# Kernel tuning notes

Measured on AMD Instinct MI355X. Metric: run time of the kernel, lower is better.

## Reference

```python
import jax, jax.numpy as jnp
import numpy as np

N = 4096; B = 32; LATENT = 16; UNITS = 64; NNZ = 65536; K = 2; M = 2 * K + 1

def _spmm(rows, cols, vals, x):
    # sparse [N,N] @ dense [N,FB] via gather + segment_sum
    return jax.ops.segment_sum(vals[:, None] * x[cols], rows, num_segments=N)

def _gconv(y, supports, W, b):
    # y: (B, N*F) -> Chebyshev-style diffusion over each support, then dense projection
    F = y.shape[1] // N
    x0 = y.reshape(B, N, F).transpose(1, 2, 0).reshape(N, F * B)
    xs = [x0]
    for rows, cols, vals in supports:
        x1 = _spmm(rows, cols, vals, x0)
        xs.append(x1)
        xk1, xk2 = x1, x0
        for _ in range(2, K + 1):
            x2 = 2.0 * _spmm(rows, cols, vals, xk1) - xk2
            xs.append(x2)
            xk1, xk2 = x2, xk1
    # [M,N,F,B] -> [B,N,F,M] -> [B*N, F*M], matching torch permute/reshape
    x = jnp.stack(xs).reshape(M, N, F, B).transpose(3, 1, 2, 0).reshape(B * N, F * M)
    return (x @ W + b).reshape(B, N * W.shape[1])

def setup_inputs():
    key = jax.random.key(0)
    ks = jax.random.split(key, 8)
    r = jax.random.randint(ks[0], (NNZ,), 0, N)
    c = jax.random.randint(ks[1], (NNZ,), 0, N)
    v = jax.random.uniform(ks[2], (NNZ,)) + 0.1
    d_row = jax.ops.segment_sum(v, r, num_segments=N)
    d_col = jax.ops.segment_sum(v, c, num_segments=N)
    inv_row = jnp.where(d_row > 0, 1.0 / d_row, 0.0)
    inv_col = jnp.where(d_col > 0, 1.0 / d_col, 0.0)
    # support1 = (D_out^{-1} A)^T ; support2 = (D_in^{-1} A^T)^T  (COO triples)
    s1_rows, s1_cols, s1_vals = c, r, v * inv_row[r]
    s2_rows, s2_cols, s2_vals = r, c, v * inv_col[c]
    def xavier(k, shape):
        scale = np.sqrt(2.0 / (shape[0] + shape[1])).astype(np.float32)
        return jax.random.normal(k, shape, dtype=jnp.float32) * scale
    return {
        "t_local": 0,
        "y": jax.random.normal(ks[3], (B, N * LATENT), dtype=jnp.float32),
        "W_theta": xavier(ks[4], (LATENT * M, LATENT)),
        "b_lat": jnp.ones((LATENT,), jnp.float32),  # bias_start=1.0; shared (LayerParams keys biases by length)
        "W_hid": xavier(ks[5], (LATENT * M, UNITS)),
        "b_hid": jnp.zeros((UNITS,), jnp.float32),
        "W_out": xavier(ks[6], (UNITS * M, LATENT)),
        "s1_rows": s1_rows, "s1_cols": s1_cols, "s1_vals": s1_vals,
        "s2_rows": s2_rows, "s2_cols": s2_cols, "s2_vals": s2_vals,
    }

def reference(t_local, y, W_theta, b_lat, W_hid, b_hid, W_out,
              s1_rows, s1_cols, s1_vals, s2_rows, s2_cols, s2_vals):
    supports = [(s1_rows, s1_cols, s1_vals), (s2_rows, s2_cols, s2_vals)]
    theta = jax.nn.sigmoid(_gconv(y, supports, W_theta, b_lat))
    c = jnp.tanh(_gconv(y, supports, W_hid, b_hid))   # gen_layers = 1
    c = jnp.tanh(_gconv(c, supports, W_out, b_lat))   # shared bias of length latent_dim
    return -theta * c
```

## Files before the change

kernel.cpp:

```cpp
#include <hip/hip_runtime.h>
#include <stdint.h>

#define NN    4096
#define BB    32
#define NNZE  65536
#define WA    512
#define WD    512

typedef __attribute__((ext_vector_type(8))) short bf16x8;
typedef __attribute__((ext_vector_type(4))) float f32x4;

__device__ __forceinline__ float bf2f_lo(unsigned int u) {
    union { unsigned int x; float f; } c; c.x = u << 16; return c.f;
}
__device__ __forceinline__ float bf2f_hi(unsigned int u) {
    union { unsigned int x; float f; } c; c.x = u & 0xffff0000u; return c.f;
}
__device__ __forceinline__ float bf2f(unsigned int h) {
    union { unsigned int u; float f; } c; c.u = h << 16; return c.f;
}
__device__ __forceinline__ unsigned int f2bf(float f) {
    union { float ff; unsigned int u; } c; c.ff = f;
    return (c.u + 0x7fffu + ((c.u >> 16) & 1u)) >> 16;
}

__global__ void hist2_kernel(const int* __restrict__ r1, const int* __restrict__ r2,
                             int* __restrict__ cnt1, int* __restrict__ cnt2) {
    int e = blockIdx.x * blockDim.x + threadIdx.x;
    if (e < NNZE) atomicAdd(&cnt1[r1[e]], 1);
    else          atomicAdd(&cnt2[r2[e - NNZE]], 1);
}

__global__ void scan2_kernel(int* cur1, int* rp1, int* cur2, int* rp2) {
    int* cur = (blockIdx.x == 0) ? cur1 : cur2;
    int* rp  = (blockIdx.x == 0) ? rp1  : rp2;
    __shared__ int part[256];
    int t = threadIdx.x;
    int base = t * 16;
    int loc[16];
    int s = 0;
#pragma unroll
    for (int i = 0; i < 16; ++i) { loc[i] = s; s += cur[base + i]; }
    part[t] = s;
    __syncthreads();
    for (int off = 1; off < 256; off <<= 1) {
        int v = 0;
        if (t >= off) v = part[t - off];
        __syncthreads();
        part[t] += v;
        __syncthreads();
    }
    int excl = (t == 0) ? 0 : part[t - 1];
#pragma unroll
    for (int i = 0; i < 16; ++i) rp[base + i] = excl + loc[i];
    __syncthreads();
#pragma unroll
    for (int i = 0; i < 16; ++i) cur[base + i] = rp[base + i];
    if (t == 255) rp[4096] = part[255];
}

__global__ void util_kernel(const int* __restrict__ r1, const int* __restrict__ c1, const float* __restrict__ v1,
                            const int* __restrict__ r2, const int* __restrict__ c2, const float* __restrict__ v2,
                            int* __restrict__ cur1, int* __restrict__ cur2,
                            int2* __restrict__ ep1, int2* __restrict__ ep2,
                            const float* __restrict__ y, unsigned short* __restrict__ x0h,
                            const float* __restrict__ Wtheta, const float* __restrict__ Whid,
                            const float* __restrict__ Wout,
                            unsigned short* __restrict__ wpa, unsigned short* __restrict__ wpo) {
    int blk = blockIdx.x, t = threadIdx.x;
    if (blk < 512) {
        int e = blk * 256 + t;
        if (e < NNZE) {
            int pos = atomicAdd(&cur1[r1[e]], 1);
            ep1[pos] = make_int2(c1[e], __float_as_int(v1[e]));
        } else {
            int ee = e - NNZE;
            int pos = atomicAdd(&cur2[r2[ee]], 1);
            ep2[pos] = make_int2(c2[ee], __float_as_int(v2[ee]));
        }
    } else if (blk < 2560) {
        int n = (blk - 512) * 2 + (t >> 7);
        int tt = t & 127;
        int b = tt & 31, q = tt >> 5;
        float4 y4 = *(const float4*)(y + (size_t)b * (NN * 16) + n * 16 + 4 * q);
        uint2 o;
        o.x = f2bf(y4.x) | (f2bf(y4.y) << 16);
        o.y = f2bf(y4.z) | (f2bf(y4.w) << 16);
        *(uint2*)(x0h + (size_t)n * WA + b * 16 + 4 * q) = o;
    } else {
        for (int i = t; i < 80 * 104; i += 256) {
            int col = i / 104, k = i - col * 104;
            float v = 0.f;
            if (k < 96) {
                int m = k >> 4, f = k & 15;
                if (m < 5) {
                    float w0, w2, w4, wm;
                    if (col < 16) {
                        w0 = Wtheta[(f * 5 + 0) * 16 + col];
                        w2 = Wtheta[(f * 5 + 2) * 16 + col];
                        w4 = Wtheta[(f * 5 + 4) * 16 + col];
                        wm = Wtheta[(f * 5 + m) * 16 + col];
                    } else {
                        int cc = col - 16;
                        w0 = Whid[(f * 5 + 0) * 64 + cc];
                        w2 = Whid[(f * 5 + 2) * 64 + cc];
                        w4 = Whid[(f * 5 + 4) * 64 + cc];
                        wm = Whid[(f * 5 + m) * 64 + cc];
                    }
                    v = (m == 0) ? w0 - w2 - w4 : (m == 2) ? 2.f * w2 : (m == 4) ? 2.f * w4 : wm;
                }
            }
            wpa[i] = (unsigned short)f2bf(v);
        }
        for (int i = t; i < 80 * 72; i += 256) {
            int col = i / 72, k = i - col * 72;
            float v = 0.f;
            if (k < 64) { int m = col >> 4, up = col & 15; v = Wout[(k * 5 + m) * 16 + up]; }
            wpo[i] = (unsigned short)f2bf(v);
        }
    }
}

__device__ __forceinline__ void gather_wave(const unsigned short* __restrict__ in,
                                            int beg, int end, const int2* __restrict__ ep,
                                            int lane, int* scol, float* sval, float* acc) {
    for (int i0 = beg; i0 < end; i0 += 64) {
        if (i0 + lane < end) { int2 e = ep[i0 + lane]; scol[lane] = e.x; sval[lane] = __int_as_float(e.y); }
        int nn = end - i0; if (nn > 64) nn = 64;
#pragma unroll 4
        for (int j = 0; j < nn; ++j) {
            const uint4* xr = (const uint4*)(in + (size_t)scol[j] * WD);
            uint4 xv = xr[lane];
            float v = sval[j];
            acc[0] += v * bf2f_lo(xv.x); acc[1] += v * bf2f_hi(xv.x);
            acc[2] += v * bf2f_lo(xv.y); acc[3] += v * bf2f_hi(xv.y);
            acc[4] += v * bf2f_lo(xv.z); acc[5] += v * bf2f_hi(xv.z);
            acc[6] += v * bf2f_lo(xv.w); acc[7] += v * bf2f_hi(xv.w);
        }
    }
}

struct SpmmDesc {
    const unsigned short* in;
    const unsigned short* prev;
    float* outF;
    unsigned short* outH;
    const int* rp; const int2* ep;
    float alpha, beta;
};

__launch_bounds__(64)
__global__ void spmmD_kernel(SpmmDesc q0, SpmmDesc q1, SpmmDesc q2, SpmmDesc q3, int ninst) {
    __shared__ int scol[64];
    __shared__ float sval[64];
    int blk = blockIdx.x;
    int xcd = blk & 7, idx = blk >> 3;
    int spx = 8 / ninst;
    int inst = xcd / spx;
    int sub  = xcd - inst * spx;
    int row  = sub * (NN / spx) + idx;
    SpmmDesc q = (inst == 0) ? q0 : (inst == 1) ? q1 : (inst == 2) ? q2 : q3;
    int lane = threadIdx.x;
    int beg = q.rp[row], end = q.rp[row + 1];
    float acc[8];
#pragma unroll
    for (int k = 0; k < 8; ++k) acc[k] = 0.f;
    gather_wave(q.in, beg, end, q.ep, lane, scol, sval, acc);
    float r[8];
#pragma unroll
    for (int k = 0; k < 8; ++k) r[k] = q.alpha * acc[k];
    if (q.prev) {
        uint4 pv = ((const uint4*)(q.prev + (size_t)row * WD))[lane];
        r[0] += q.beta * bf2f_lo(pv.x); r[1] += q.beta * bf2f_hi(pv.x);
        r[2] += q.beta * bf2f_lo(pv.y); r[3] += q.beta * bf2f_hi(pv.y);
        r[4] += q.beta * bf2f_lo(pv.z); r[5] += q.beta * bf2f_hi(pv.z);
        r[6] += q.beta * bf2f_lo(pv.w); r[7] += q.beta * bf2f_hi(pv.w);
    }
    if (q.outF) {
        float* po = q.outF + (size_t)row * WD + lane * 8;
        *(float4*)(po)     = make_float4(r[0], r[1], r[2], r[3]);
        *(float4*)(po + 4) = make_float4(r[4], r[5], r[6], r[7]);
    } else {
        uint4 o;
        o.x = f2bf(r[0]) | (f2bf(r[1]) << 16);
        o.y = f2bf(r[2]) | (f2bf(r[3]) << 16);
        o.z = f2bf(r[4]) | (f2bf(r[5]) << 16);
        o.w = f2bf(r[6]) | (f2bf(r[7]) << 16);
        ((uint4*)(q.outH + (size_t)row * WD))[lane] = o;
    }
}

__launch_bounds__(256)
__global__ void proj_fused(const unsigned short* __restrict__ xh,
                           const unsigned short* __restrict__ wpa,
                           const unsigned short* __restrict__ wpo,
                           const float* __restrict__ b_hid,
                           float* __restrict__ theta,
                           float* __restrict__ d0,
                           unsigned short* __restrict__ dd1, unsigned short* __restrict__ dd2,
                           unsigned short* __restrict__ dd3, unsigned short* __restrict__ dd4) {
    __shared__ __align__(16) unsigned short sWa[80 * 104];
    __shared__ __align__(16) unsigned short sWo[80 * 72];
    __shared__ __align__(16) unsigned short sC[4][32 * 72];
    int t = threadIdx.x;
    for (int i = t; i < 1040; i += 256) ((uint4*)sWa)[i] = ((const uint4*)wpa)[i];
    for (int i = t; i < 720; i += 256) ((uint4*)sWo)[i] = ((const uint4*)wpo)[i];
    __syncthreads();
    int lane = t & 63, w = t >> 6;
    int r = lane & 15, g = lane >> 4;
    bf16x8 wfa[5][3];
#pragma unroll
    for (int ct = 0; ct < 5; ++ct)
#pragma unroll
        for (int kt = 0; kt < 3; ++kt)
            wfa[ct][kt] = *(const bf16x8*)(sWa + (ct * 16 + r) * 104 + kt * 32 + g * 8);
    float bh[4];
#pragma unroll
    for (int ct = 0; ct < 4; ++ct) bh[ct] = b_hid[ct * 16 + r];
    unsigned short* myC = (unsigned short*)sC[w];

    for (int i = 0; i < 2; ++i) {
        int n = blockIdx.x * 8 + w * 2 + i;
        f32x4 acc[2][5];
#pragma unroll
        for (int bt = 0; bt < 2; ++bt)
#pragma unroll
            for (int ct = 0; ct < 5; ++ct)
                acc[bt][ct] = (f32x4){0.f, 0.f, 0.f, 0.f};
#pragma unroll
        for (int kt = 0; kt < 3; ++kt) {
            bf16x8 a[2];
            int m = kt * 2 + (g >> 1);
#pragma unroll
            for (int bt = 0; bt < 2; ++bt) {
                bf16x8 av = {0, 0, 0, 0, 0, 0, 0, 0};
                if (m < 5)
                    av = *(const bf16x8*)(xh + ((size_t)m * NN + n) * WA
                                          + (bt * 16 + r) * 16 + (g & 1) * 8);
                a[bt] = av;
            }
#pragma unroll
            for (int bt = 0; bt < 2; ++bt)
#pragma unroll
                for (int ct = 0; ct < 5; ++ct)
                    acc[bt][ct] = __builtin_amdgcn_mfma_f32_16x16x32_bf16(
                        a[bt], wfa[ct][kt], acc[bt][ct], 0, 0, 0);
        }
#pragma unroll
        for (int bt = 0; bt < 2; ++bt) {
#pragma unroll
            for (int reg = 0; reg < 4; ++reg) {
                int b = bt * 16 + g * 4 + reg;
                theta[(size_t)n * 512 + b * 16 + r] = acc[bt][0][reg];
            }
#pragma unroll
            for (int ct = 1; ct < 5; ++ct) {
                int u = (ct - 1) * 16 + r;
#pragma unroll
                for (int reg = 0; reg < 4; ++reg) {
                    int b = bt * 16 + g * 4 + reg;
                    myC[b * 72 + u] = (unsigned short)f2bf(tanhf(acc[bt][ct][reg] + bh[ct - 1]));
                }
            }
        }
        f32x4 acc2[2][5];
#pragma unroll
        for (int bt = 0; bt < 2; ++bt)
#pragma unroll
            for (int ct = 0; ct < 5; ++ct)
                acc2[bt][ct] = (f32x4){0.f, 0.f, 0.f, 0.f};
#pragma unroll
        for (int kt = 0; kt < 2; ++kt) {
            bf16x8 a2[2];
#pragma unroll
            for (int bt = 0; bt < 2; ++bt)
                a2[bt] = *(const bf16x8*)(myC + (bt * 16 + r) * 72 + kt * 32 + g * 8);
#pragma unroll
            for (int ct = 0; ct < 5; ++ct) {
                bf16x8 wo = *(const bf16x8*)(sWo + (ct * 16 + r) * 72 + kt * 32 + g * 8);
#pragma unroll
                for (int bt = 0; bt < 2; ++bt)
                    acc2[bt][ct] = __builtin_amdgcn_mfma_f32_16x16x32_bf16(
                        a2[bt], wo, acc2[bt][ct], 0, 0, 0);
            }
        }
#pragma unroll
        for (int bt = 0; bt < 2; ++bt) {
#pragma unroll
            for (int reg = 0; reg < 4; ++reg) {
                int b = bt * 16 + g * 4 + reg;
                d0[(size_t)n * WD + b * 16 + r] = acc2[bt][0][reg];
            }
#pragma unroll
            for (int ct = 1; ct < 5; ++ct) {
                unsigned short* dp = (ct == 1) ? dd1 : (ct == 2) ? dd2 : (ct == 3) ? dd3 : dd4;
#pragma unroll
                for (int reg = 0; reg < 4; ++reg) {
                    int b = bt * 16 + g * 4 + reg;
                    dp[(size_t)n * WD + b * 16 + r] = (unsigned short)f2bf(acc2[bt][ct][reg]);
                }
            }
        }
    }
}

__launch_bounds__(64)
__global__ void finalspmm_kernel(const unsigned short* __restrict__ g1, const unsigned short* __restrict__ g3,
                                 const int* __restrict__ rp1, const int2* __restrict__ ep1,
                                 const int* __restrict__ rp2, const int2* __restrict__ ep2,
                                 const float* __restrict__ theta, const float* __restrict__ d0,
                                 const unsigned short* __restrict__ dd2, const unsigned short* __restrict__ dd4,
                                 const float* __restrict__ b_lat, float* __restrict__ out) {
    __shared__ int scol[64];
    __shared__ float sval[64];
    int blk = blockIdx.x;
    int row = (blk & 7) * 512 + (blk >> 3);
    int lane = threadIdx.x;
    float h[8];
#pragma unroll
    for (int k = 0; k < 8; ++k) h[k] = 0.f;
    gather_wave(g1, rp1[row], rp1[row + 1], ep1, lane, scol, sval, h);
    gather_wave(g3, rp2[row], rp2[row + 1], ep2, lane, scol, sval, h);
    size_t base = (size_t)row * WD + lane * 8;
    float4 dA = *(const float4*)(d0 + base);
    float4 dB = *(const float4*)(d0 + base + 4);
    uint4 p2 = *(const uint4*)(dd2 + base);
    uint4 p4 = *(const uint4*)(dd4 + base);
    float4 tA = *(const float4*)(theta + base);
    float4 tB = *(const float4*)(theta + base + 4);
    float4 blA = *(const float4*)(b_lat + (lane & 1) * 8);
    float4 blB = *(const float4*)(b_lat + (lane & 1) * 8 + 4);
    float tot[8], th[8];
    tot[0] = dA.x - bf2f_lo(p2.x) - bf2f_lo(p4.x) + h[0] + blA.x;
    tot[1] = dA.y - bf2f_hi(p2.x) - bf2f_hi(p4.x) + h[1] + blA.y;
    tot[2] = dA.z - bf2f_lo(p2.y) - bf2f_lo(p4.y) + h[2] + blA.z;
    tot[3] = dA.w - bf2f_hi(p2.y) - bf2f_hi(p4.y) + h[3] + blA.w;
    tot[4] = dB.x - bf2f_lo(p2.z) - bf2f_lo(p4.z) + h[4] + blB.x;
    tot[5] = dB.y - bf2f_hi(p2.z) - bf2f_hi(p4.z) + h[5] + blB.y;
    tot[6] = dB.z - bf2f_lo(p2.w) - bf2f_lo(p4.w) + h[6] + blB.z;
    tot[7] = dB.w - bf2f_hi(p2.w) - bf2f_hi(p4.w) + h[7] + blB.w;
    th[0] = tA.x + blA.x; th[1] = tA.y + blA.y; th[2] = tA.z + blA.z; th[3] = tA.w + blA.w;
    th[4] = tB.x + blB.x; th[5] = tB.y + blB.y; th[6] = tB.z + blB.z; th[7] = tB.w + blB.w;
    float res[8];
#pragma unroll
    for (int j = 0; j < 8; ++j)
        res[j] = -(1.f / (1.f + expf(-th[j]))) * tanhf(tot[j]);
    float* po = out + ((size_t)(lane >> 1) * NN + row) * 16 + (lane & 1) * 8;
    *(float4*)(po)     = make_float4(res[0], res[1], res[2], res[3]);
    *(float4*)(po + 4) = make_float4(res[4], res[5], res[6], res[7]);
}

extern "C" void kernel_launch(void* const* d_in, const int* in_sizes, int n_in,
                              void* d_out, int out_size, void* d_ws, size_t ws_size,
                              hipStream_t stream) {
    const float* y      = (const float*)d_in[1];
    const float* Wtheta = (const float*)d_in[2];
    const float* b_lat  = (const float*)d_in[3];
    const float* Whid   = (const float*)d_in[4];
    const float* b_hid  = (const float*)d_in[5];
    const float* Wout   = (const float*)d_in[6];
    const int*   r1     = (const int*)d_in[7];
    const int*   c1     = (const int*)d_in[8];
    const float* v1     = (const float*)d_in[9];
    const int*   r2     = (const int*)d_in[10];
    const int*   c2     = (const int*)d_in[11];
    const float* v2     = (const float*)d_in[12];
    float* out = (float*)d_out;

    char* ws = (char*)d_ws;
    size_t off = 0;
    auto alloc = [&](size_t bytes) -> char* {
        char* p = ws + off;
        off += (bytes + 255) & ~(size_t)255;
        return p;
    };
    int*   rp1   = (int*)alloc(4097 * 4);
    int*   rp2   = (int*)alloc(4097 * 4);
    int*   cur1  = (int*)alloc(4096 * 4);
    int*   cur2  = (int*)alloc(4096 * 4);
    int2*  ep1   = (int2*)alloc((size_t)NNZE * 8);
    int2*  ep2   = (int2*)alloc((size_t)NNZE * 8);
    unsigned short* wpa = (unsigned short*)alloc(80 * 104 * 2);
    unsigned short* wpo = (unsigned short*)alloc(80 * 72 * 2);
    unsigned short* xh = (unsigned short*)alloc((size_t)5 * NN * WA * 2);
    float* theta = (float*)alloc((size_t)NN * 512 * 4);
    float* d0    = (float*)alloc((size_t)NN * WD * 4);
    unsigned short* dd1 = (unsigned short*)alloc((size_t)NN * WD * 2);
    unsigned short* dd2 = (unsigned short*)alloc((size_t)NN * WD * 2);
    unsigned short* dd3 = (unsigned short*)alloc((size_t)NN * WD * 2);
    unsigned short* dd4 = (unsigned short*)alloc((size_t)NN * WD * 2);
    unsigned short* g1  = (unsigned short*)alloc((size_t)NN * WD * 2);
    unsigned short* g3  = (unsigned short*)alloc((size_t)NN * WD * 2);
    if (off > ws_size) return;

    unsigned short* x0h = xh;
    unsigned short* x1h = xh + (size_t)1 * NN * WA;
    unsigned short* x2h = xh + (size_t)2 * NN * WA;
    unsigned short* x3h = xh + (size_t)3 * NN * WA;
    unsigned short* x4h = xh + (size_t)4 * NN * WA;

    hipMemsetAsync(cur1, 0, 2 * 4096 * 4, stream);
    hist2_kernel<<<2 * NNZE / 256, 256, 0, stream>>>(r1, r2, cur1, cur2);
    scan2_kernel<<<2, 256, 0, stream>>>(cur1, rp1, cur2, rp2);
    util_kernel<<<2561, 256, 0, stream>>>(r1, c1, v1, r2, c2, v2, cur1, cur2, ep1, ep2,
                                          y, x0h, Wtheta, Whid, Wout, wpa, wpo);

    {
        SpmmDesc a0 = { x0h, nullptr, nullptr, x1h, rp1, ep1, 1.f, 0.f };
        SpmmDesc a1 = { x0h, nullptr, nullptr, x3h, rp2, ep2, 1.f, 0.f };
        spmmD_kernel<<<2 * NN, 64, 0, stream>>>(a0, a1, a0, a1, 2);
    }
    {
        SpmmDesc a0 = { x1h, nullptr, nullptr, x2h, rp1, ep1, 1.f, 0.f };
        SpmmDesc a1 = { x3h, nullptr, nullptr, x4h, rp2, ep2, 1.f, 0.f };
        spmmD_kernel<<<2 * NN, 64, 0, stream>>>(a0, a1, a0, a1, 2);
    }

    proj_fused<<<NN / 8, 256, 0, stream>>>(xh, wpa, wpo, b_hid,
                                           theta, d0, dd1, dd2, dd3, dd4);

    {
        SpmmDesc a0 = { dd2, dd1, nullptr, g1, rp1, ep1, 2.f, 1.f };
        SpmmDesc a1 = { dd4, dd3, nullptr, g3, rp2, ep2, 2.f, 1.f };
        spmmD_kernel<<<2 * NN, 64, 0, stream>>>(a0, a1, a0, a1, 2);
    }
    finalspmm_kernel<<<NN, 64, 0, stream>>>(g1, g3, rp1, ep1, rp2, ep2,
                                            theta, d0, dd2, dd4, b_lat, out);
}
```

Measured before the change: 204.4 us.

## Fuse all stages into one cooperative persistent kernel with grid syncs

Replaces the chain of seven launches (histogram, scan, util, three SpMM passes, projection, final SpMM) with a single cooperative kernel of 512 blocks that runs each stage in turn, separated by grid.sync(). The aim is to remove launch gaps and tail effects between the short dependent stages. The edge list now stores column indices premultiplied by the row stride, which saves a multiply per gather. If a cooperative launch is unsupported or fails, it falls back to the old multi-kernel path. In exchange it adds grid-barrier cost and gives each stage fewer concurrent waves than the previous 8192-wave SpMM grids.

After: 204.0 us. Within noise of the previous version (-0.2%).

```diff
diff --git a/kernel.cpp b/kernel.cpp
--- a/kernel.cpp
+++ b/kernel.cpp
@@ -1,11 +1,15 @@
 #include <hip/hip_runtime.h>
+#include <hip/hip_cooperative_groups.h>
 #include <stdint.h>
+
+namespace cg = cooperative_groups;
 
 #define NN    4096
 #define BB    32
 #define NNZE  65536
 #define WA    512
 #define WD    512
+#define MGRID 512
 
 typedef __attribute__((ext_vector_type(8))) short bf16x8;
 typedef __attribute__((ext_vector_type(4))) float f32x4;
@@ -24,18 +28,8 @@
     return (c.u + 0x7fffu + ((c.u >> 16) & 1u)) >> 16;
 }
 
-__global__ void hist2_kernel(const int* __restrict__ r1, const int* __restrict__ r2,
-                             int* __restrict__ cnt1, int* __restrict__ cnt2) {
-    int e = blockIdx.x * blockDim.x + threadIdx.x;
-    if (e < NNZE) atomicAdd(&cnt1[r1[e]], 1);
-    else          atomicAdd(&cnt2[r2[e - NNZE]], 1);
-}
-
-__global__ void scan2_kernel(int* cur1, int* rp1, int* cur2, int* rp2) {
-    int* cur = (blockIdx.x == 0) ? cur1 : cur2;
-    int* rp  = (blockIdx.x == 0) ? rp1  : rp2;
-    __shared__ int part[256];
-    int t = threadIdx.x;
+
+__device__ __forceinline__ void scan_dev(int* cur, int* rp, int* part, int t) {
     int base = t * 16;
     int loc[16];
     int s = 0;
@@ -59,65 +53,48 @@
     if (t == 255) rp[4096] = part[255];
 }
 
-__global__ void util_kernel(const int* __restrict__ r1, const int* __restrict__ c1, const float* __restrict__ v1,
-                            const int* __restrict__ r2, const int* __restrict__ c2, const float* __restrict__ v2,
-                            int* __restrict__ cur1, int* __restrict__ cur2,
-                            int2* __restrict__ ep1, int2* __restrict__ ep2,
-                            const float* __restrict__ y, unsigned short* __restrict__ x0h,
-                            const float* __restrict__ Wtheta, const float* __restrict__ Whid,
-                            const float* __restrict__ Wout,
-                            unsigned short* __restrict__ wpa, unsigned short* __restrict__ wpo) {
-    int blk = blockIdx.x, t = threadIdx.x;
-    if (blk < 512) {
-        int e = blk * 256 + t;
-        if (e < NNZE) {
-            int pos = atomicAdd(&cur1[r1[e]], 1);
-            ep1[pos] = make_int2(c1[e], __float_as_int(v1[e]));
-        } else {
-            int ee = e - NNZE;
-            int pos = atomicAdd(&cur2[r2[ee]], 1);
-            ep2[pos] = make_int2(c2[ee], __float_as_int(v2[ee]));
-        }
-    } else if (blk < 2560) {
-        int n = (blk - 512) * 2 + (t >> 7);
-        int tt = t & 127;
-        int b = tt & 31, q = tt >> 5;
-        float4 y4 = *(const float4*)(y + (size_t)b * (NN * 16) + n * 16 + 4 * q);
-        uint2 o;
-        o.x = f2bf(y4.x) | (f2bf(y4.y) << 16);
-        o.y = f2bf(y4.z) | (f2bf(y4.w) << 16);
-        *(uint2*)(x0h + (size_t)n * WA + b * 16 + 4 * q) = o;
-    } else {
-        for (int i = t; i < 80 * 104; i += 256) {
-            int col = i / 104, k = i - col * 104;
-            float v = 0.f;
-            if (k < 96) {
-                int m = k >> 4, f = k & 15;
-                if (m < 5) {
-                    float w0, w2, w4, wm;
-                    if (col < 16) {
-                        w0 = Wtheta[(f * 5 + 0) * 16 + col];
-                        w2 = Wtheta[(f * 5 + 2) * 16 + col];
-                        w4 = Wtheta[(f * 5 + 4) * 16 + col];
-                        wm = Wtheta[(f * 5 + m) * 16 + col];
-                    } else {
-                        int cc = col - 16;
-                        w0 = Whid[(f * 5 + 0) * 64 + cc];
-                        w2 = Whid[(f * 5 + 2) * 64 + cc];
-                        w4 = Whid[(f * 5 + 4) * 64 + cc];
-                        wm = Whid[(f * 5 + m) * 64 + cc];
-                    }
-                    v = (m == 0) ? w0 - w2 - w4 : (m == 2) ? 2.f * w2 : (m == 4) ? 2.f * w4 : wm;
+__device__ __forceinline__ void transA_item(int item, const float* y, unsigned short* x0h) {
+    int n = item >> 7, tt = item & 127;
+    int b = tt & 31, q = tt >> 5;
+    float4 y4 = *(const float4*)(y + (size_t)b * (NN * 16) + n * 16 + 4 * q);
+    uint2 o;
+    o.x = f2bf(y4.x) | (f2bf(y4.y) << 16);
+    o.y = f2bf(y4.z) | (f2bf(y4.w) << 16);
+    *(uint2*)(x0h + (size_t)n * WA + b * 16 + 4 * q) = o;
+}
+
+__device__ __forceinline__ void prep_dev(int t, const float* Wtheta, const float* Whid,
+                                         const float* Wout,
+                                         unsigned short* wpa, unsigned short* wpo) {
+    for (int i = t; i < 80 * 104; i += 256) {
+        int col = i / 104, k = i - col * 104;
+        float v = 0.f;
+        if (k < 96) {
+            int m = k >> 4, f = k & 15;
+            if (m < 5) {
+                float w0, w2, w4, wm;
+                if (col < 16) {
+                    w0 = Wtheta[(f * 5 + 0) * 16 + col];
+                    w2 = Wtheta[(f * 5 + 2) * 16 + col];
+                    w4 = Wtheta[(f * 5 + 4) * 16 + col];
+                    wm = Wtheta[(f * 5 + m) * 16 + col];
+                } else {
+                    int cc = col - 16;
+                    w0 = Whid[(f * 5 + 0) * 64 + cc];
+                    w2 = Whid[(f * 5 + 2) * 64 + cc];
+                    w4 = Whid[(f * 5 + 4) * 64 + cc];
+                    wm = Whid[(f * 5 + m) * 64 + cc];
                 }
+                v = (m == 0) ? w0 - w2 - w4 : (m == 2) ? 2.f * w2 : (m == 4) ? 2.f * w4 : wm;
             }
-            wpa[i] = (unsigned short)f2bf(v);
-        }
-        for (int i = t; i < 80 * 72; i += 256) {
-            int col = i / 72, k = i - col * 72;
-            float v = 0.f;
-            if (k < 64) { int m = col >> 4, up = col & 15; v = Wout[(k * 5 + m) * 16 + up]; }
-            wpo[i] = (unsigned short)f2bf(v);
-        }
+        }
+        wpa[i] = (unsigned short)f2bf(v);
+    }
+    for (int i = t; i < 80 * 72; i += 256) {
+        int col = i / 72, k = i - col * 72;
+        float v = 0.f;
+        if (k < 64) { int m = col >> 4, up = col & 15; v = Wout[(k * 5 + m) * 16 + up]; }
+        wpo[i] = (unsigned short)f2bf(v);
     }
 }
 
@@ -129,7 +106,7 @@
         int nn = end - i0; if (nn > 64) nn = 64;
 #pragma unroll 4
         for (int j = 0; j < nn; ++j) {
-            const uint4* xr = (const uint4*)(in + (size_t)scol[j] * WD);
+            const uint4* xr = (const uint4*)(in + scol[j]);
             uint4 xv = xr[lane];
             float v = sval[j];
             acc[0] += v * bf2f_lo(xv.x); acc[1] += v * bf2f_hi(xv.x);
@@ -140,182 +117,129 @@
     }
 }
 
-struct SpmmDesc {
-    const unsigned short* in;
-    const unsigned short* prev;
-    float* outF;
-    unsigned short* outH;
-    const int* rp; const int2* ep;
-    float alpha, beta;
-};
-
-__launch_bounds__(64)
-__global__ void spmmD_kernel(SpmmDesc q0, SpmmDesc q1, SpmmDesc q2, SpmmDesc q3, int ninst) {
-    __shared__ int scol[64];
-    __shared__ float sval[64];
-    int blk = blockIdx.x;
-    int xcd = blk & 7, idx = blk >> 3;
-    int spx = 8 / ninst;
-    int inst = xcd / spx;
-    int sub  = xcd - inst * spx;
-    int row  = sub * (NN / spx) + idx;
-    SpmmDesc q = (inst == 0) ? q0 : (inst == 1) ? q1 : (inst == 2) ? q2 : q3;
-    int lane = threadIdx.x;
-    int beg = q.rp[row], end = q.rp[row + 1];
+__device__ __forceinline__ void spmm_row(const unsigned short* in, const unsigned short* prev,
+                                         unsigned short* outH,
+                                         const int* rp, const int2* ep, float alpha, float beta,
+                                         int row, int lane, int* scol, float* sval) {
+    int beg = rp[row], end = rp[row + 1];
     float acc[8];
 #pragma unroll
     for (int k = 0; k < 8; ++k) acc[k] = 0.f;
-    gather_wave(q.in, beg, end, q.ep, lane, scol, sval, acc);
+    gather_wave(in, beg, end, ep, lane, scol, sval, acc);
     float r[8];
 #pragma unroll
-    for (int k = 0; k < 8; ++k) r[k] = q.alpha * acc[k];
-    if (q.prev) {
-        uint4 pv = ((const uint4*)(q.prev + (size_t)row * WD))[lane];
-        r[0] += q.beta * bf2f_lo(pv.x); r[1] += q.beta * bf2f_hi(pv.x);
-        r[2] += q.beta * bf2f_lo(pv.y); r[3] += q.beta * bf2f_hi(pv.y);
-        r[4] += q.beta * bf2f_lo(pv.z); r[5] += q.beta * bf2f_hi(pv.z);
-        r[6] += q.beta * bf2f_lo(pv.w); r[7] += q.beta * bf2f_hi(pv.w);
-    }
-    if (q.outF) {
-        float* po = q.outF + (size_t)row * WD + lane * 8;
-        *(float4*)(po)     = make_float4(r[0], r[1], r[2], r[3]);
-        *(float4*)(po + 4) = make_float4(r[4], r[5], r[6], r[7]);
-    } else {
-        uint4 o;
-        o.x = f2bf(r[0]) | (f2bf(r[1]) << 16);
-        o.y = f2bf(r[2]) | (f2bf(r[3]) << 16);
-        o.z = f2bf(r[4]) | (f2bf(r[5]) << 16);
-        o.w = f2bf(r[6]) | (f2bf(r[7]) << 16);
-        ((uint4*)(q.outH + (size_t)row * WD))[lane] = o;
-    }
-}
-
-__launch_bounds__(256)
-__global__ void proj_fused(const unsigned short* __restrict__ xh,
-                           const unsigned short* __restrict__ wpa,
-                           const unsigned short* __restrict__ wpo,
-                           const float* __restrict__ b_hid,
-                           float* __restrict__ theta,
-                           float* __restrict__ d0,
-                           unsigned short* __restrict__ dd1, unsigned short* __restrict__ dd2,
-                           unsigned short* __restrict__ dd3, unsigned short* __restrict__ dd4) {
-    __shared__ __align__(16) unsigned short sWa[80 * 104];
-    __shared__ __align__(16) unsigned short sWo[80 * 72];
-    __shared__ __align__(16) unsigned short sC[4][32 * 72];
-    int t = threadIdx.x;
-    for (int i = t; i < 1040; i += 256) ((uint4*)sWa)[i] = ((const uint4*)wpa)[i];
-    for (int i = t; i < 720; i += 256) ((uint4*)sWo)[i] = ((const uint4*)wpo)[i];
-    __syncthreads();
-    int lane = t & 63, w = t >> 6;
-    int r = lane & 15, g = lane >> 4;
-    bf16x8 wfa[5][3];
-#pragma unroll
-    for (int ct = 0; ct < 5; ++ct)
-#pragma unroll
-        for (int kt = 0; kt < 3; ++kt)
-            wfa[ct][kt] = *(const bf16x8*)(sWa + (ct * 16 + r) * 104 + kt * 32 + g * 8);
-    float bh[4];
-#pragma unroll
-    for (int ct = 0; ct < 4; ++ct) bh[ct] = b_hid[ct * 16 + r];
-    unsigned short* myC = (unsigned short*)sC[w];
-
-    for (int i = 0; i < 2; ++i) {
-        int n = blockIdx.x * 8 + w * 2 + i;
-        f32x4 acc[2][5];
+    for (int k = 0; k < 8; ++k) r[k] = alpha * acc[k];
+    if (prev) {
+        uint4 pv = ((const uint4*)(prev + (size_t)row * WD))[lane];
+        r[0] += beta * bf2f_lo(pv.x); r[1] += beta * bf2f_hi(pv.x);
+        r[2] += beta * bf2f_lo(pv.y); r[3] += beta * bf2f_hi(pv.y);
+        r[4] += beta * bf2f_lo(pv.z); r[5] += beta * bf2f_hi(pv.z);
+        r[6] += beta * bf2f_lo(pv.w); r[7] += beta * bf2f_hi(pv.w);
+    }
+    uint4 o;
+    o.x = f2bf(r[0]) | (f2bf(r[1]) << 16);
+    o.y = f2bf(r[2]) | (f2bf(r[3]) << 16);
+    o.z = f2bf(r[4]) | (f2bf(r[5]) << 16);
+    o.w = f2bf(r[6]) | (f2bf(r[7]) << 16);
+    ((uint4*)(outH + (size_t)row * WD))[lane] = o;
+}
+
+__device__ __forceinline__ void proj_one(int n, int r, int g,
+                                         const bf16x8 (&wfa)[5][3], const float (&bh)[4],
+                                         const unsigned short* sWo, unsigned short* myC,
+                                         const unsigned short* xh,
+                                         float* theta, float* d0,
+                                         unsigned short* dd1, unsigned short* dd2,
+                                         unsigned short* dd3, unsigned short* dd4) {
+    f32x4 acc[2][5];
+#pragma unroll
+    for (int bt = 0; bt < 2; ++bt)
+#pragma unroll
+        for (int ct = 0; ct < 5; ++ct)
+            acc[bt][ct] = (f32x4){0.f, 0.f, 0.f, 0.f};
+#pragma unroll
+    for (int kt = 0; kt < 3; ++kt) {
+        bf16x8 a[2];
+        int m = kt * 2 + (g >> 1);
+#pragma unroll
+        for (int bt = 0; bt < 2; ++bt) {
+            bf16x8 av = {0, 0, 0, 0, 0, 0, 0, 0};
+            if (m < 5)
+                av = *(const bf16x8*)(xh + ((size_t)m * NN + n) * WA
+                                      + (bt * 16 + r) * 16 + (g & 1) * 8);
+            a[bt] = av;
+        }
 #pragma unroll
         for (int bt = 0; bt < 2; ++bt)
 #pragma unroll
             for (int ct = 0; ct < 5; ++ct)
-                acc[bt][ct] = (f32x4){0.f, 0.f, 0.f, 0.f};
-#pragma unroll
-        for (int kt = 0; kt < 3; ++kt) {
-            bf16x8 a[2];
-            int m = kt * 2 + (g >> 1);
-#pragma unroll
-            for (int bt = 0; bt < 2; ++bt) {
-                bf16x8 av = {0, 0, 0, 0, 0, 0, 0, 0};
-                if (m < 5)
-                    av = *(const bf16x8*)(xh + ((size_t)m * NN + n) * WA
-                                          + (bt * 16 + r) * 16 + (g & 1) * 8);
-                a[bt] = av;
-            }
-#pragma unroll
-            for (int bt = 0; bt < 2; ++bt)
-#pragma unroll
-                for (int ct = 0; ct < 5; ++ct)
-                    acc[bt][ct] = __builtin_amdgcn_mfma_f32_16x16x32_bf16(
-                        a[bt], wfa[ct][kt], acc[bt][ct], 0, 0, 0);
-        }
-#pragma unroll
-        for (int bt = 0; bt < 2; ++bt) {
+                acc[bt][ct] = __builtin_amdgcn_mfma_f32_16x16x32_bf16(
+                    a[bt], wfa[ct][kt], acc[bt][ct], 0, 0, 0);
+    }
+#pragma unroll
+    for (int bt = 0; bt < 2; ++bt) {
+#pragma unroll
+        for (int reg = 0; reg < 4; ++reg) {
+            int b = bt * 16 + g * 4 + reg;
+            theta[(size_t)n * 512 + b * 16 + r] = acc[bt][0][reg];
+        }
+#pragma unroll
+        for (int ct = 1; ct < 5; ++ct) {
+            int u = (ct - 1) * 16 + r;
 #pragma unroll
             for (int reg = 0; reg < 4; ++reg) {
                 int b = bt * 16 + g * 4 + reg;
-                theta[(size_t)n * 512 + b * 16 + r] = acc[bt][0][reg];
+                myC[b * 72 + u] = (unsigned short)f2bf(tanhf(acc[bt][ct][reg] + bh[ct - 1]));
             }
-#pragma unroll
-            for (int ct = 1; ct < 5; ++ct) {
-                int u = (ct - 1) * 16 + r;
-#pragma unroll
-                for (int reg = 0; reg < 4; ++reg) {
-                    int b = bt * 16 + g * 4 + reg;
-                    myC[b * 72 + u] = (unsigned short)f2bf(tanhf(acc[bt][ct][reg] + bh[ct - 1]));
-                }
-            }
-        }
-        f32x4 acc2[2][5];
+        }
+    }
+    f32x4 acc2[2][5];
+#pragma unroll
+    for (int bt = 0; bt < 2; ++bt)
+#pragma unroll
+        for (int ct = 0; ct < 5; ++ct)
+            acc2[bt][ct] = (f32x4){0.f, 0.f, 0.f, 0.f};
+#pragma unroll
+    for (int kt = 0; kt < 2; ++kt) {
+        bf16x8 a2[2];
 #pragma unroll
         for (int bt = 0; bt < 2; ++bt)
-#pragma unroll
-            for (int ct = 0; ct < 5; ++ct)
-                acc2[bt][ct] = (f32x4){0.f, 0.f, 0.f, 0.f};
-#pragma unroll
-        for (int kt = 0; kt < 2; ++kt) {
-            bf16x8 a2[2];
+            a2[bt] = *(const bf16x8*)(myC + (bt * 16 + r) * 72 + kt * 32 + g * 8);
+#pragma unroll
+        for (int ct = 0; ct < 5; ++ct) {
+            bf16x8 wo = *(const bf16x8*)(sWo + (ct * 16 + r) * 72 + kt * 32 + g * 8);
 #pragma unroll
             for (int bt = 0; bt < 2; ++bt)
-                a2[bt] = *(const bf16x8*)(myC + (bt * 16 + r) * 72 + kt * 32 + g * 8);
-#pragma unroll
-            for (int ct = 0; ct < 5; ++ct) {
-                bf16x8 wo = *(const bf16x8*)(sWo + (ct * 16 + r) * 72 + kt * 32 + g * 8);
-#pragma unroll
-                for (int bt = 0; bt < 2; ++bt)
-                    acc2[bt][ct] = __builtin_amdgcn_mfma_f32_16x16x32_bf16(
-                        a2[bt], wo, acc2[bt][ct], 0, 0, 0);
-            }
-        }
-#pragma unroll
-        for (int bt = 0; bt < 2; ++bt) {
+                acc2[bt][ct] = __builtin_amdgcn_mfma_f32_16x16x32_bf16(
+                    a2[bt], wo, acc2[bt][ct], 0, 0, 0);
+        }
+    }
+#pragma unroll
+    for (int bt = 0; bt < 2; ++bt) {
+#pragma unroll
+        for (int reg = 0; reg < 4; ++reg) {
+            int b = bt * 16 + g * 4 + reg;
+            d0[(size_t)n * WD + b * 16 + r] = acc2[bt][0][reg];
+        }
+#pragma unroll
+        for (int ct = 1; ct < 5; ++ct) {
+            unsigned short* dp = (ct == 1) ? dd1 : (ct == 2) ? dd2 : (ct == 3) ? dd3 : dd4;
 #pragma unroll
             for (int reg = 0; reg < 4; ++reg) {
                 int b = bt * 16 + g * 4 + reg;
-                d0[(size_t)n * WD + b * 16 + r] = acc2[bt][0][reg];
+                dp[(size_t)n * WD + b * 16 + r] = (unsigned short)f2bf(acc2[bt][ct][reg]);
             }
-#pragma unroll
-            for (int ct = 1; ct < 5; ++ct) {
-                unsigned short* dp = (ct == 1) ? dd1 : (ct == 2) ? dd2 : (ct == 3) ? dd3 : dd4;
-#pragma unroll
-                for (int reg = 0; reg < 4; ++reg) {
-                    int b = bt * 16 + g * 4 + reg;
-                    dp[(size_t)n * WD + b * 16 + r] = (unsigned short)f2bf(acc2[bt][ct][reg]);
-                }
-            }
-        }
-    }
-}
-
-__launch_bounds__(64)
-__global__ void finalspmm_kernel(const unsigned short* __restrict__ g1, const unsigned short* __restrict__ g3,
-                                 const int* __restrict__ rp1, const int2* __restrict__ ep1,
-                                 const int* __restrict__ rp2, const int2* __restrict__ ep2,
-                                 const float* __restrict__ theta, const float* __restrict__ d0,
-                                 const unsigned short* __restrict__ dd2, const unsigned short* __restrict__ dd4,
-                                 const float* __restrict__ b_lat, float* __restrict__ out) {
-    __shared__ int scol[64];
-    __shared__ float sval[64];
-    int blk = blockIdx.x;
-    int row = (blk & 7) * 512 + (blk >> 3);
-    int lane = threadIdx.x;
+        }
+    }
+}
+
+__device__ __forceinline__ void final_row(int row, int lane, int* scol, float* sval,
+                                          const unsigned short* g1, const unsigned short* g3,
+                                          const int* rp1, const int2* ep1,
+                                          const int* rp2, const int2* ep2,
+                                          const float* theta, const float* d0,
+                                          const unsigned short* dd2, const unsigned short* dd4,
+                                          const float* b_lat, float* out) {
     float h[8];
 #pragma unroll
     for (int k = 0; k < 8; ++k) h[k] = 0.f;
@@ -349,6 +273,229 @@
     *(float4*)(po)     = make_float4(res[0], res[1], res[2], res[3]);
     *(float4*)(po + 4) = make_float4(res[4], res[5], res[6], res[7]);
 }
+
+
+struct MegaArgs {
+    const int *r1, *c1; const float* v1;
+    const int *r2, *c2; const float* v2;
+    int *cur1, *cur2, *rp1, *rp2;
+    int2 *ep1, *ep2;
+    const float *y, *Wtheta, *Whid, *Wout, *b_hid, *b_lat;
+    unsigned short *x0h, *x1h, *x2h, *x3h, *x4h, *wpa, *wpo;
+    float *theta, *d0;
+    unsigned short *dd1, *dd2, *dd3, *dd4, *g1, *g3;
+    float* out;
+};
+
+__launch_bounds__(256, 2)
+__global__ void mega_kernel(MegaArgs a) {
+    cg::grid_group grid = cg::this_grid();
+    __shared__ int part[256];
+    __shared__ int  sscol[4][64];
+    __shared__ float ssval[4][64];
+    __shared__ __align__(16) unsigned short sWa[80 * 104];
+    __shared__ __align__(16) unsigned short sWo[80 * 72];
+    __shared__ __align__(16) unsigned short sC[4][32 * 72];
+    int blk = blockIdx.x, t = threadIdx.x;
+    int w = t >> 6, lane = t & 63;
+    int gw = blk * 4 + w;
+    int* scol = sscol[w];
+    float* sval = ssval[w];
+
+    {
+        int e = blk * 256 + t;
+        if (e < NNZE) atomicAdd(&a.cur1[a.r1[e]], 1);
+        else          atomicAdd(&a.cur2[a.r2[e - NNZE]], 1);
+    }
+    grid.sync();
+    if (blk < 2) scan_dev(blk == 0 ? a.cur1 : a.cur2, blk == 0 ? a.rp1 : a.rp2, part, t);
+    grid.sync();
+    {
+        int e = blk * 256 + t;
+        if (e < NNZE) {
+            int pos = atomicAdd(&a.cur1[a.r1[e]], 1);
+            a.ep1[pos] = make_int2(a.c1[e] * WD, __float_as_int(a.v1[e]));
+        } else {
+            int ee = e - NNZE;
+            int pos = atomicAdd(&a.cur2[a.r2[ee]], 1);
+            a.ep2[pos] = make_int2(a.c2[ee] * WD, __float_as_int(a.v2[ee]));
+        }
+#pragma unroll
+        for (int rep = 0; rep < 4; ++rep)
+            transA_item(e + rep * 131072, a.y, a.x0h);
+        if (blk == MGRID - 1) prep_dev(t, a.Wtheta, a.Whid, a.Wout, a.wpa, a.wpo);
+    }
+    grid.sync();
+    {
+        int xcd = blk & 7, inst = xcd >> 2, sub = xcd & 3;
+        int local = (blk >> 3) * 4 + w;
+#pragma unroll
+        for (int rr = 0; rr < 4; ++rr) {
+            int row = sub * 1024 + local * 4 + rr;
+            if (inst == 0) spmm_row(a.x0h, nullptr, a.x1h, a.rp1, a.ep1, 1.f, 0.f, row, lane, scol, sval);
+            else           spmm_row(a.x0h, nullptr, a.x3h, a.rp2, a.ep2, 1.f, 0.f, row, lane, scol, sval);
+        }
+    }
+    grid.sync();
+    {
+        int xcd = blk & 7, inst = xcd >> 2, sub = xcd & 3;
+        int local = (blk >> 3) * 4 + w;
+#pragma unroll
+        for (int rr = 0; rr < 4; ++rr) {
+            int row = sub * 1024 + local * 4 + rr;
+            if (inst == 0) spmm_row(a.x1h, nullptr, a.x2h, a.rp1, a.ep1, 1.f, 0.f, row, lane, scol, sval);
+            else           spmm_row(a.x3h, nullptr, a.x4h, a.rp2, a.ep2, 1.f, 0.f, row, lane, scol, sval);
+        }
+    }
+    grid.sync();
+    {
+        for (int i = t; i < 1040; i += 256) ((uint4*)sWa)[i] = ((const uint4*)a.wpa)[i];
+        for (int i = t; i < 720; i += 256) ((uint4*)sWo)[i] = ((const uint4*)a.wpo)[i];
+        __syncthreads();
+        int r = lane & 15, g = lane >> 4;
+        bf16x8 wfa[5][3];
+#pragma unroll
+        for (int ct = 0; ct < 5; ++ct)
+#pragma unroll
+            for (int kt = 0; kt < 3; ++kt)
+                wfa[ct][kt] = *(const bf16x8*)(sWa + (ct * 16 + r) * 104 + kt * 32 + g * 8);
+        float bh[4];
+#pragma unroll
+        for (int ct = 0; ct < 4; ++ct) bh[ct] = a.b_hid[ct * 16 + r];
+        unsigned short* myC = (unsigned short*)sC[w];
+        for (int i = 0; i < 2; ++i)
+            proj_one(gw * 2 + i, r, g, wfa, bh, sWo, myC, a.x0h,
+                     a.theta, a.d0, a.dd1, a.dd2, a.dd3, a.dd4);
+    }
+    grid.sync();
+    {
+        int xcd = blk & 7, inst = xcd >> 2, sub = xcd & 3;
+        int local = (blk >> 3) * 4 + w;
+#pragma unroll
+        for (int rr = 0; rr < 4; ++rr) {
+            int row = sub * 1024 + local * 4 + rr;
+            if (inst == 0) spmm_row(a.dd2, a.dd1, a.g1, a.rp1, a.ep1, 2.f, 1.f, row, lane, scol, sval);
+            else           spmm_row(a.dd4, a.dd3, a.g3, a.rp2, a.ep2, 2.f, 1.f, row, lane, scol, sval);
+        }
+    }
+    grid.sync();
+    {
+        int local = (blk >> 3) * 4 + w;
+#pragma unroll
+        for (int rr = 0; rr < 2; ++rr) {
+            int row = (blk & 7) * 512 + local * 2 + rr;
+            final_row(row, lane, scol, sval, a.g1, a.g3, a.rp1, a.ep1, a.rp2, a.ep2,
+                      a.theta, a.d0, a.dd2, a.dd4, a.b_lat, a.out);
+        }
+    }
+}
+
+
+__global__ void hist2_kernel(const int* __restrict__ r1, const int* __restrict__ r2,
+                             int* __restrict__ cnt1, int* __restrict__ cnt2) {
+    int e = blockIdx.x * blockDim.x + threadIdx.x;
+    if (e < NNZE) atomicAdd(&cnt1[r1[e]], 1);
+    else          atomicAdd(&cnt2[r2[e - NNZE]], 1);
+}
+
+__global__ void scan2_kernel(int* cur1, int* rp1, int* cur2, int* rp2) {
+    __shared__ int part[256];
+    scan_dev(blockIdx.x == 0 ? cur1 : cur2, blockIdx.x == 0 ? rp1 : rp2, part, threadIdx.x);
+}
+
+__global__ void util_kernel(const int* __restrict__ r1, const int* __restrict__ c1, const float* __restrict__ v1,
+                            const int* __restrict__ r2, const int* __restrict__ c2, const float* __restrict__ v2,
+                            int* __restrict__ cur1, int* __restrict__ cur2,
+                            int2* __restrict__ ep1, int2* __restrict__ ep2,
+                            const float* __restrict__ y, unsigned short* __restrict__ x0h,
+                            const float* __restrict__ Wtheta, const float* __restrict__ Whid,
+                            const float* __restrict__ Wout,
+                            unsigned short* __restrict__ wpa, unsigned short* __restrict__ wpo) {
+    int blk = blockIdx.x, t = threadIdx.x;
+    if (blk < 512) {
+        int e = blk * 256 + t;
+        if (e < NNZE) {
+            int pos = atomicAdd(&cur1[r1[e]], 1);
+            ep1[pos] = make_int2(c1[e] * WD, __float_as_int(v1[e]));
+        } else {
+            int ee = e - NNZE;
+            int pos = atomicAdd(&cur2[r2[ee]], 1);
+            ep2[pos] = make_int2(c2[ee] * WD, __float_as_int(v2[ee]));
+        }
+    } else if (blk < 2560) {
+        transA_item((blk - 512) * 256 + t, y, x0h);
+    } else {
+        prep_dev(t, Wtheta, Whid, Wout, wpa, wpo);
+    }
+}
+
+struct SpmmDesc {
+    const unsigned short* in;
+    const unsigned short* prev;
+    unsigned short* outH;
+    const int* rp; const int2* ep;
+    float alpha, beta;
+};
+
+__launch_bounds__(64)
+__global__ void spmmD_kernel(SpmmDesc q0, SpmmDesc q1) {
+    __shared__ int scol[64];
+    __shared__ float sval[64];
+    int blk = blockIdx.x;
+    int xcd = blk & 7, idx = blk >> 3;
+    int inst = xcd >> 2, sub = xcd & 3;
+    int row = sub * 1024 + idx;
+    const SpmmDesc& q = inst == 0 ? q0 : q1;
+    spmm_row(q.in, q.prev, q.outH, q.rp, q.ep, q.alpha, q.beta, row, threadIdx.x, scol, sval);
+}
+
+__launch_bounds__(256)
+__global__ void proj_fused(const unsigned short* __restrict__ xh,
+                           const unsigned short* __restrict__ wpa,
+                           const unsigned short* __restrict__ wpo,
+                           const float* __restrict__ b_hid,
+                           float* __restrict__ theta, float* __restrict__ d0,
+                           unsigned short* __restrict__ dd1, unsigned short* __restrict__ dd2,
+                           unsigned short* __restrict__ dd3, unsigned short* __restrict__ dd4) {
+    __shared__ __align__(16) unsigned short sWa[80 * 104];
+    __shared__ __align__(16) unsigned short sWo[80 * 72];
+    __shared__ __align__(16) unsigned short sC[4][32 * 72];
+    int t = threadIdx.x;
+    for (int i = t; i < 1040; i += 256) ((uint4*)sWa)[i] = ((const uint4*)wpa)[i];
+    for (int i = t; i < 720; i += 256) ((uint4*)sWo)[i] = ((const uint4*)wpo)[i];
+    __syncthreads();
+    int lane = t & 63, w = t >> 6;
+    int r = lane & 15, g = lane >> 4;
+    bf16x8 wfa[5][3];
+#pragma unroll
+    for (int ct = 0; ct < 5; ++ct)
+#pragma unroll
+        for (int kt = 0; kt < 3; ++kt)
+            wfa[ct][kt] = *(const bf16x8*)(sWa + (ct * 16 + r) * 104 + kt * 32 + g * 8);
+    float bh[4];
+#pragma unroll
+    for (int ct = 0; ct < 4; ++ct) bh[ct] = b_hid[ct * 16 + r];
+    unsigned short* myC = (unsigned short*)sC[w];
+    for (int i = 0; i < 2; ++i)
+        proj_one(blockIdx.x * 8 + w * 2 + i, r, g, wfa, bh, sWo, myC, xh,
+                 theta, d0, dd1, dd2, dd3, dd4);
+}
+
+__launch_bounds__(64)
+__global__ void finalspmm_kernel(const unsigned short* __restrict__ g1, const unsigned short* __restrict__ g3,
+                                 const int* __restrict__ rp1, const int2* __restrict__ ep1,
+                                 const int* __restrict__ rp2, const int2* __restrict__ ep2,
+                                 const float* __restrict__ theta, const float* __restrict__ d0,
+                                 const unsigned short* __restrict__ dd2, const unsigned short* __restrict__ dd4,
+                                 const float* __restrict__ b_lat, float* __restrict__ out) {
+    __shared__ int scol[64];
+    __shared__ float sval[64];
+    int blk = blockIdx.x;
+    int row = (blk & 7) * 512 + (blk >> 3);
+    final_row(row, threadIdx.x, scol, sval, g1, g3, rp1, ep1, rp2, ep2,
+              theta, d0, dd2, dd4, b_lat, out);
+}
+
 
 extern "C" void kernel_launch(void* const* d_in, const int* in_sizes, int n_in,
                               void* d_out, int out_size, void* d_ws, size_t ws_size,
@@ -400,29 +547,50 @@
     unsigned short* x4h = xh + (size_t)4 * NN * WA;
 
     hipMemsetAsync(cur1, 0, 2 * 4096 * 4, stream);
+
+    static int coop_state = -1;
+    if (coop_state == -1) {
+        int dev = 0, coopAttr = 0, nCU = 0, maxPerCU = 0;
+        hipGetDevice(&dev);
+        hipDeviceGetAttribute(&coopAttr, hipDeviceAttributeCooperativeLaunch, dev);
+        hipDeviceGetAttribute(&nCU, hipDeviceAttributeMultiprocessorCount, dev);
+        hipError_t oe = hipOccupancyMaxActiveBlocksPerMultiprocessor(&maxPerCU, mega_kernel, 256, 0);
+        coop_state = (coopAttr && oe == hipSuccess && maxPerCU * nCU >= MGRID) ? 1 : 0;
+    }
+    bool ran_coop = false;
+    if (coop_state == 1) {
+        MegaArgs ma = { r1, c1, v1, r2, c2, v2, cur1, cur2, rp1, rp2, ep1, ep2,
+                        y, Wtheta, Whid, Wout, b_hid, b_lat,
+                        x0h, x1h, x2h, x3h, x4h, wpa, wpo,
+                        theta, d0, dd1, dd2, dd3, dd4, g1, g3, out };
+        void* kp[] = { &ma };
+        hipError_t le = hipLaunchCooperativeKernel((const void*)mega_kernel,
+                                                   dim3(MGRID), dim3(256), kp, 0, stream);
+        if (le == hipSuccess) ran_coop = true;
+        else coop_state = 0;
+    }
+    if (ran_coop) return;
+
     hist2_kernel<<<2 * NNZE / 256, 256, 0, stream>>>(r1, r2, cur1, cur2);
     scan2_kernel<<<2, 256, 0, stream>>>(cur1, rp1, cur2, rp2);
     util_kernel<<<2561, 256, 0, stream>>>(r1, c1, v1, r2, c2, v2, cur1, cur2, ep1, ep2,
                                           y, x0h, Wtheta, Whid, Wout, wpa, wpo);
-
-    {
-        SpmmDesc a0 = { x0h, nullptr, nullptr, x1h, rp1, ep1, 1.f, 0.f };
-        SpmmDesc a1 = { x0h, nullptr, nullptr, x3h, rp2, ep2, 1.f, 0.f };
-        spmmD_kernel<<<2 * NN, 64, 0, stream>>>(a0, a1, a0, a1, 2);
-    }
-    {
-        SpmmDesc a0 = { x1h, nullptr, nullptr, x2h, rp1, ep1, 1.f, 0.f };
-        SpmmDesc a1 = { x3h, nullptr, nullptr, x4h, rp2, ep2, 1.f, 0.f };
-        spmmD_kernel<<<2 * NN, 64, 0, stream>>>(a0, a1, a0, a1, 2);
-    }
-
+    {
+        SpmmDesc a0 = { x0h, nullptr, x1h, rp1, ep1, 1.f, 0.f };
+        SpmmDesc a1 = { x0h, nullptr, x3h, rp2, ep2, 1.f, 0.f };
+        spmmD_kernel<<<2 * NN, 64, 0, stream>>>(a0, a1);
+    }
+    {
+        SpmmDesc a0 = { x1h, nullptr, x2h, rp1, ep1, 1.f, 0.f };
+        SpmmDesc a1 = { x3h, nullptr, x4h, rp2, ep2, 1.f, 0.f };
+        spmmD_kernel<<<2 * NN, 64, 0, stream>>>(a0, a1);
+    }
     proj_fused<<<NN / 8, 256, 0, stream>>>(xh, wpa, wpo, b_hid,
                                            theta, d0, dd1, dd2, dd3, dd4);
-
-    {
-        SpmmDesc a0 = { dd2, dd1, nullptr, g1, rp1, ep1, 2.f, 1.f };
-        SpmmDesc a1 = { dd4, dd3, nullptr, g3, rp2, ep2, 2.f, 1.f };
-        spmmD_kernel<<<2 * NN, 64, 0, stream>>>(a0, a1, a0, a1, 2);
+    {
+        SpmmDesc a0 = { dd2, dd1, g1, rp1, ep1, 2.f, 1.f };
+        SpmmDesc a1 = { dd4, dd3, g3, rp2, ep2, 2.f, 1.f };
+        spmmD_kernel<<<2 * NN, 64, 0, stream>>>(a0, a1);
     }
     finalspmm_kernel<<<NN, 64, 0, stream>>>(g1, g3, rp1, ep1, rp2, ep2,
                                             theta, d0, dd2, dd4, b_lat, out);
```
